# Performance work log

Measured on AMD Instinct MI355X. Metric: run time of the kernel, lower is better.

The kernel has to match this reference:

```python
import jax, jax.numpy as jnp
import numpy as np

H = 12
D_MODEL = 768
D_K = D_MODEL // H  # 64


def setup_inputs() -> dict:
    key = jax.random.key(0)
    ks = jax.random.split(key, 16)
    B, S, D = 4, 1024, D_MODEL
    scale = 1.0 / np.sqrt(D)
    inp = {
        "query": jax.random.normal(ks[0], (B, S, D), jnp.float32),
        "key": jax.random.normal(ks[1], (B, S, D), jnp.float32),
        "value": jax.random.normal(ks[2], (B, S, D), jnp.float32),
        "times": jax.random.normal(ks[3], (2, B, S, D), jnp.float32),
        # learned params (Linear weights stored torch-style [out, in])
        "Wq": jax.random.normal(ks[4], (D, D), jnp.float32) * scale,
        "bq": jnp.zeros((D,), jnp.float32),
        "Wk": jax.random.normal(ks[5], (D, D), jnp.float32) * scale,
        "bk": jnp.zeros((D,), jnp.float32),
        "Wv": jax.random.normal(ks[6], (D, D), jnp.float32) * scale,
        "bv": jnp.zeros((D,), jnp.float32),
        "Wt": jax.random.normal(ks[7], (D, D), jnp.float32) * scale,
        "bt": jnp.zeros((D,), jnp.float32),
        "Wo": jax.random.normal(ks[8], (D, D), jnp.float32) * scale,
        "bo": jnp.zeros((D,), jnp.float32),
    }
    return inp


def _split_heads(x, B, S):
    # [B,S,D] -> [B,H,S,D_K]
    return x.reshape(B, S, H, D_K).transpose(0, 2, 1, 3)


def reference(query, key, value, times, Wq, bq, Wk, bk, Wv, bv, Wt, bt, Wo, bo):
    B, S, D = query.shape
    inv_sqrt_dk = 1.0 / jnp.sqrt(jnp.asarray(D_K, query.dtype))
    # q/k/v projections are identical across time-loop iterations; hoist them.
    q = _split_heads(query @ Wq.T + bq, B, S)   # [B,H,S,dk]
    k = _split_heads(key @ Wk.T + bk, B, S)
    v = _split_heads(value @ Wv.T + bv, B, S)
    x = jnp.zeros_like(q)
    n_times = times.shape[0]
    for i in range(n_times):  # small fixed loop over time embeddings
        t = _split_heads(times[i] @ Wt.T + bt, B, S)
        # dual-score attention: query.time + query.key, each scaled by 1/sqrt(d_k)
        scores = (jnp.einsum('bhqd,bhkd->bhqk', q, t)
                  + jnp.einsum('bhqd,bhkd->bhqk', q, k)) * inv_sqrt_dk
        p = jax.nn.softmax(scores, axis=-1)
        x = x + jnp.einsum('bhqk,bhkd->bhqd', p, v)
    x = x.transpose(0, 2, 1, 3).reshape(B, S, H * D_K)
    return x @ Wo.T + bo
```

## Files before the change

### kernel.cpp

```cpp
#include <hip/hip_runtime.h>
#include <hip/hip_fp16.h>

typedef _Float16 v8h __attribute__((ext_vector_type(8)));
typedef _Float16 v4h __attribute__((ext_vector_type(4)));
typedef _Float16 v2h __attribute__((ext_vector_type(2)));
typedef float v4f __attribute__((ext_vector_type(4)));

#define MFMA_F16 __builtin_amdgcn_mfma_f32_16x16x32_f16
#define EXP2F __builtin_amdgcn_exp2f

__device__ static inline v2h pkrtz(float a, float b) {
  return __builtin_bit_cast(v2h, __builtin_amdgcn_cvt_pkrtz(a, b));
}

__device__ static inline void async_copy16(const void* g, void* l) {
  __builtin_amdgcn_global_load_lds(
      (const __attribute__((address_space(1))) void*)g,
      (__attribute__((address_space(3))) void*)l, 16, 0, 0);
}

struct CastArgs {
  const float* src[5];
  _Float16* dst[5];
  int start[6];
  float scale[5];
};
__global__ void cast_all(CastArgs a) {
  const int g = blockIdx.x * 256 + threadIdx.x;
  if (g >= a.start[5]) return;
  int z = 0;
  #pragma unroll
  for (int i = 1; i < 5; ++i) if (g >= a.start[i]) z = i;
  const int i0 = g - a.start[z];
  const float sc = a.scale[z];
  const float* s = a.src[z] + (size_t)i0 * 8;
  const float4 f0 = *(const float4*)s;
  const float4 f1 = *(const float4*)(s + 4);
  v8h o = {(_Float16)(f0.x * sc), (_Float16)(f0.y * sc),
           (_Float16)(f0.z * sc), (_Float16)(f0.w * sc),
           (_Float16)(f1.x * sc), (_Float16)(f1.y * sc),
           (_Float16)(f1.z * sc), (_Float16)(f1.w * sc)};
  *(v8h*)(a.dst[z] + (size_t)i0 * 8) = o;
}

struct GemmArgs {
  const void* A1[4]; const void* A2[4];
  const _Float16* W1[4]; const _Float16* W2[4];
  const float* b1[4];    const float* b2[4];
  void* out[4];
  float bscale[4];
  int K[4];
  int mode[4];
};

template <int MT, bool AF32>
__global__ __launch_bounds__(256) void gemm_mt(GemmArgs g) {
  constexpr int NMT = MT / 32;
  constexpr int ASLOT = MT / 32;
  __shared__ _Float16 a_lds[(AF32 ? 1 : 2) * MT * 64];
  __shared__ _Float16 w_lds[2 * 128 * 64];
  const int z = blockIdx.z;
  const int KK = g.K[z];
  const int tid = threadIdx.x;
  const int w = tid >> 6, lane = tid & 63, quad = lane >> 4, l16 = lane & 15;
  const int m0 = blockIdx.x * MT, n0 = blockIdx.y * 128;
  const int wm = (w >> 1) * (MT / 2), wn = (w & 1) * 64;

  size_t srcOffW[4]; int ldsOffW[4];
  #pragma unroll
  for (int i = 0; i < 4; ++i) {
    const int c = i * 256 + tid, row = c >> 3, slot = c & 7;
    srcOffW[i] = (size_t)row * 768 + (size_t)((slot ^ (row & 7)) * 8);
    ldsOffW[i] = (i * 256 + w * 64) * 8;
  }

  auto stageW = [&](const _Float16* Wsrc, int kc, int buf) {
    #pragma unroll
    for (int i = 0; i < 4; ++i)
      async_copy16(Wsrc + (size_t)n0 * 768 + kc + srcOffW[i],
                   &w_lds[buf * 8192 + ldsOffW[i]]);
  };
  auto stageA16 = [&](const _Float16* Asrc, int kc, int buf) {
    #pragma unroll
    for (int i = 0; i < MT / 32; ++i)
      async_copy16(Asrc + (size_t)m0 * 768 + kc + srcOffW[i],
                   &a_lds[buf * MT * 64 + ldsOffW[i]]);
  };

  int rowA[ASLOT], colA[ASLOT], dstA[ASLOT];
  float4 areg[ASLOT][2];
  if constexpr (AF32) {
    #pragma unroll
    for (int i = 0; i < ASLOT; ++i) {
      const int s = i * 256 + tid, row = s >> 3, slot = s & 7;
      rowA[i] = row;
      colA[i] = (slot ^ (row & 7)) * 8;
      dstA[i] = s * 8;
    }
  }
  auto loadA = [&](const float* Af, int kc) {
    #pragma unroll
    for (int i = 0; i < ASLOT; ++i) {
      const float* p = Af + (size_t)(m0 + rowA[i]) * 768 + kc + colA[i];
      areg[i][0] = *(const float4*)p;
      areg[i][1] = *(const float4*)(p + 4);
    }
  };
  auto writeA = [&]() {
    #pragma unroll
    for (int i = 0; i < ASLOT; ++i) {
      const float4 f0 = areg[i][0], f1 = areg[i][1];
      v8h o = {(_Float16)f0.x, (_Float16)f0.y, (_Float16)f0.z, (_Float16)f0.w,
               (_Float16)f1.x, (_Float16)f1.y, (_Float16)f1.z, (_Float16)f1.w};
      *(v8h*)&a_lds[dstA[i]] = o;
    }
  };

  const void* A1 = g.A1[z]; const void* A2 = g.A2[z];
  const _Float16* W1 = g.W1[z]; const _Float16* W2 = g.W2[z];

  v4f acc[NMT][4] = {};

  if constexpr (AF32) loadA((const float*)A1, 0);
  else stageA16((const _Float16*)A1, 0, 0);
  stageW(W1, 0, 0);

  int cur = 0;
  for (int k0 = 0; k0 < KK; k0 += 64) {
    const int k0n = k0 + 64;
    const bool has_next = k0n < KK;
    const int kcn = (k0n < 768) ? k0n : k0n - 768;
    const bool nfirst = k0n < 768;

    __syncthreads();

    if constexpr (AF32) {
      writeA();
      __syncthreads();
      if (has_next) {
        loadA((const float*)(nfirst ? A1 : A2), kcn);
        stageW(nfirst ? W1 : W2, kcn, cur ^ 1);
      }
    } else {
      if (has_next) {
        stageA16((const _Float16*)(nfirst ? A1 : A2), kcn, cur ^ 1);
        stageW(nfirst ? W1 : W2, kcn, cur ^ 1);
      }
    }

    const _Float16* al;
    if constexpr (AF32) al = a_lds; else al = &a_lds[cur * MT * 64];
    const _Float16* wl = &w_lds[cur * 8192];

    #pragma unroll
    for (int kh = 0; kh < 2; ++kh) {
      v8h af[NMT], bf[4];
      #pragma unroll
      for (int mt = 0; mt < NMT; ++mt) {
        const int r = wm + mt * 16 + l16;
        af[mt] = *(const v8h*)&al[r * 64 + (((kh * 4 + quad) ^ (r & 7)) * 8)];
      }
      #pragma unroll
      for (int nt = 0; nt < 4; ++nt) {
        const int r = wn + nt * 16 + l16;
        bf[nt] = *(const v8h*)&wl[r * 64 + (((kh * 4 + quad) ^ (r & 7)) * 8)];
      }
      #pragma unroll
      for (int mt = 0; mt < NMT; ++mt)
        #pragma unroll
        for (int nt = 0; nt < 4; ++nt)
          acc[mt][nt] = MFMA_F16(af[mt], bf[nt], acc[mt][nt], 0, 0, 0);
    }
    cur ^= 1;
  }

  const int mode = g.mode[z];
  #pragma unroll
  for (int nt = 0; nt < 4; ++nt) {
    const int col = n0 + wn + nt * 16 + l16;
    float bv = g.b1[z][col] * g.bscale[z];
    if (g.b2[z]) bv += g.b2[z][col];
    if (mode == 1) {
      _Float16* outp = (_Float16*)g.out[z];
      const int h = col >> 6, dk = col & 63;
      #pragma unroll
      for (int mt = 0; mt < NMT; ++mt) {
        const int row = m0 + wm + mt * 16 + quad * 4;
        const int b = row >> 10, s = row & 1023;
        const int sp = (s & ~31) | ((s & 12) << 1) | ((s & 16) >> 2);
        v4h pack = {(_Float16)(acc[mt][nt][0] + bv), (_Float16)(acc[mt][nt][1] + bv),
                    (_Float16)(acc[mt][nt][2] + bv), (_Float16)(acc[mt][nt][3] + bv)};
        *(v4h*)&outp[(size_t)((b * 12 + h) * 64 + dk) * 1024 + sp] = pack;
      }
    } else {
      #pragma unroll
      for (int mt = 0; mt < NMT; ++mt)
        #pragma unroll
        for (int r = 0; r < 4; ++r) {
          const int row = m0 + wm + mt * 16 + quad * 4 + r;
          const float v = acc[mt][nt][r] + bv;
          if (mode == 2) ((float*)g.out[z])[(size_t)row * 768 + col] = v;
          else ((_Float16*)g.out[z])[(size_t)row * 768 + col] = (_Float16)v;
        }
    }
  }
}

__global__ __launch_bounds__(256) void attn(
    const _Float16* __restrict__ Q,
    const _Float16* __restrict__ KT0, const _Float16* __restrict__ KT1,
    const _Float16* __restrict__ Vt,
    _Float16* __restrict__ X)
{
  __shared__ _Float16 lds[6 * 4096];

  const int tid = threadIdx.x;
  const int w = tid >> 6, lane = tid & 63, quad = lane >> 4, l16 = lane & 15;

  const int orig = blockIdx.y * 16 + blockIdx.x;
  const int wgid = (orig & 7) * 96 + (orig >> 3);
  const int bh = wgid >> 4, q0 = (wgid & 15) * 64;
  const int b = bh / 12, h = bh % 12;
  const size_t base = (size_t)b * 1024 * 768 + h * 64;

  const _Float16* k0s = KT0 + base;
  const _Float16* k1s = KT1 + base;
  const _Float16* vs  = Vt + (size_t)bh * 64 * 1024;

  size_t ktOff[2], vOff[2]; int ldsOff[2];
  #pragma unroll
  for (int i = 0; i < 2; ++i) {
    const int c = i * 256 + w * 64 + lane, row = c >> 3, slot = c & 7;
    const int logical = slot ^ (row & 7);
    ktOff[i] = (size_t)row * 768 + (size_t)(logical * 8);
    vOff[i] = (size_t)row * 1024 + (size_t)(logical * 8);
    ldsOff[i] = c * 8;
  }
  auto stage = [&](int buf) {
    #pragma unroll
    for (int i = 0; i < 2; ++i) {
      async_copy16(k0s + ktOff[i], &lds[buf * 4096 + ldsOff[i]]);
      async_copy16(k1s + ktOff[i], &lds[8192 + buf * 4096 + ldsOff[i]]);
      async_copy16(vs + vOff[i], &lds[16384 + buf * 4096 + ldsOff[i]]);
    }
    k0s += 64 * 768; k1s += 64 * 768; vs += 64;
  };

  const _Float16* Qw = Q + base + (size_t)(q0 + w * 16) * 768;
  const v8h qf0 = *(const v8h*)(Qw + (size_t)l16 * 768 + quad * 8);
  const v8h qf1 = *(const v8h*)(Qw + (size_t)l16 * 768 + 32 + quad * 8);

  int ra0[4], ra1[4];
  #pragma unroll
  for (int t = 0; t < 4; ++t) {
    const int r = t * 16 + l16, rw = r & 7;
    ra0[t] = (r * 64 + ((quad ^ rw) * 8)) * 2;
    ra1[t] = ra0[t] ^ 64;
  }

  const _Float16 one = (_Float16)1.f;
  const v8h ones8 = {one, one, one, one, one, one, one, one};
  v4f o[2][4] = {};
  v4f osum[2] = {};

  auto body = [&](int B, bool doStage) {
    __syncthreads();
    if (doStage) stage((B == 0) ? 1 : 0);

    const char* L = (const char*)lds;

    v4f s[2][4];
    __builtin_amdgcn_s_setprio(1);
    #pragma unroll
    for (int kvt = 0; kvt < 4; ++kvt) {
      const v8h k00 = *(const v8h*)(L + B + ra0[kvt]);
      const v8h k01 = *(const v8h*)(L + B + ra1[kvt]);
      const v8h k10 = *(const v8h*)(L + 16384 + B + ra0[kvt]);
      const v8h k11 = *(const v8h*)(L + 16384 + B + ra1[kvt]);
      s[0][kvt] = MFMA_F16(k00, qf0, v4f{}, 0, 0, 0);
      s[0][kvt] = MFMA_F16(k01, qf1, s[0][kvt], 0, 0, 0);
      s[1][kvt] = MFMA_F16(k10, qf0, v4f{}, 0, 0, 0);
      s[1][kvt] = MFMA_F16(k11, qf1, s[1][kvt], 0, 0, 0);
    }
    __builtin_amdgcn_s_setprio(0);

    v8h pb8[2][2];
    #pragma unroll
    for (int t = 0; t < 2; ++t)
      #pragma unroll
      for (int gg = 0; gg < 2; ++gg) {
        const v4f sa = s[t][gg * 2], sb = s[t][gg * 2 + 1];
        const v2h a0 = pkrtz(EXP2F(sa[0]), EXP2F(sa[1]));
        const v2h a1 = pkrtz(EXP2F(sa[2]), EXP2F(sa[3]));
        const v2h b0 = pkrtz(EXP2F(sb[0]), EXP2F(sb[1]));
        const v2h b1 = pkrtz(EXP2F(sb[2]), EXP2F(sb[3]));
        pb8[t][gg] = v8h{a0[0], a0[1], a1[0], a1[1], b0[0], b0[1], b1[0], b1[1]};
        osum[t] = MFMA_F16(ones8, pb8[t][gg], osum[t], 0, 0, 0);
      }

    __builtin_amdgcn_s_setprio(1);
    #pragma unroll
    for (int dkt = 0; dkt < 4; ++dkt) {
      const v8h v0 = *(const v8h*)(L + 32768 + B + ra0[dkt]);
      const v8h v1 = *(const v8h*)(L + 32768 + B + ra1[dkt]);
      o[0][dkt] = MFMA_F16(v0, pb8[0][0], o[0][dkt], 0, 0, 0);
      o[0][dkt] = MFMA_F16(v1, pb8[0][1], o[0][dkt], 0, 0, 0);
      o[1][dkt] = MFMA_F16(v0, pb8[1][0], o[1][dkt], 0, 0, 0);
      o[1][dkt] = MFMA_F16(v1, pb8[1][1], o[1][dkt], 0, 0, 0);
    }
    __builtin_amdgcn_s_setprio(0);
  };

  stage(0);
  for (int it = 0; it < 7; ++it) {
    body(0, true);
    body(8192, true);
  }
  body(0, true);
  body(8192, false);

  const float i0 = 1.0f / osum[0][0], i1 = 1.0f / osum[1][0];

  _Float16* Xw = X + base + (size_t)(q0 + w * 16 + l16) * 768;
  #pragma unroll
  for (int dkt = 0; dkt < 4; ++dkt) {
    v4h pack;
    #pragma unroll
    for (int r = 0; r < 4; ++r)
      pack[r] = (_Float16)(o[0][dkt][r] * i0 + o[1][dkt][r] * i1);
    *(v4h*)&Xw[dkt * 16 + quad * 4] = pack;
  }
}

extern "C" void kernel_launch(void* const* d_in, const int* in_sizes, int n_in,
                              void* d_out, int out_size, void* d_ws, size_t ws_size,
                              hipStream_t stream) {
  const float* query = (const float*)d_in[0];
  const float* key   = (const float*)d_in[1];
  const float* value = (const float*)d_in[2];
  const float* times = (const float*)d_in[3];
  const float* Wq = (const float*)d_in[4];  const float* bq = (const float*)d_in[5];
  const float* Wk = (const float*)d_in[6];  const float* bk = (const float*)d_in[7];
  const float* Wv = (const float*)d_in[8];  const float* bv = (const float*)d_in[9];
  const float* Wt = (const float*)d_in[10]; const float* bt = (const float*)d_in[11];
  const float* Wo = (const float*)d_in[12]; const float* bo = (const float*)d_in[13];
  float* out = (float*)d_out;

  const size_t NELEM = (size_t)4096 * 768;
  const size_t WELEM = (size_t)768 * 768;
  const float QSCALE = 0.125f * 1.4426950408889634f;

  char* ws = (char*)d_ws;
  size_t off = 0;
  auto alloc = [&](size_t bytes) {
    void* p = ws + off; off += (bytes + 255) & ~(size_t)255; return p;
  };
  _Float16* wqh = (_Float16*)alloc(WELEM * 2);
  _Float16* wkh = (_Float16*)alloc(WELEM * 2);
  _Float16* wvh = (_Float16*)alloc(WELEM * 2);
  _Float16* wth = (_Float16*)alloc(WELEM * 2);
  _Float16* woh = (_Float16*)alloc(WELEM * 2);
  _Float16* Qh  = (_Float16*)alloc(NELEM * 2);
  _Float16* KT0 = (_Float16*)alloc(NELEM * 2);
  _Float16* KT1 = (_Float16*)alloc(NELEM * 2);
  _Float16* Vt  = (_Float16*)alloc(NELEM * 2);
  _Float16* Xh  = (_Float16*)alloc(NELEM * 2);

  CastArgs ca = {};
  const int nW8 = (int)(WELEM / 8);
  const float* csrc[5] = {Wq, Wk, Wv, Wt, Wo};
  _Float16* cdst[5] = {wqh, wkh, wvh, wth, woh};
  int acc8 = 0;
  for (int i = 0; i < 5; ++i) {
    ca.src[i] = csrc[i]; ca.dst[i] = cdst[i];
    ca.start[i] = acc8;
    acc8 += nW8;
    ca.scale[i] = (i == 0) ? QSCALE : 1.0f;
  }
  ca.start[5] = acc8;
  cast_all<<<dim3((acc8 + 255) / 256), 256, 0, stream>>>(ca);

  GemmArgs pa = {};
  pa.A1[0] = times;         pa.A2[0] = key; pa.W1[0] = wth; pa.W2[0] = wkh;
  pa.b1[0] = bt; pa.b2[0] = bk; pa.out[0] = KT0; pa.bscale[0] = 1.0f;
  pa.K[0] = 1536; pa.mode[0] = 0;
  pa.A1[1] = times + NELEM; pa.A2[1] = key; pa.W1[1] = wth; pa.W2[1] = wkh;
  pa.b1[1] = bt; pa.b2[1] = bk; pa.out[1] = KT1; pa.bscale[1] = 1.0f;
  pa.K[1] = 1536; pa.mode[1] = 0;
  pa.A1[2] = query; pa.A2[2] = query; pa.W1[2] = wqh; pa.W2[2] = wqh;
  pa.b1[2] = bq; pa.b2[2] = nullptr; pa.out[2] = Qh; pa.bscale[2] = QSCALE;
  pa.K[2] = 768; pa.mode[2] = 0;
  pa.A1[3] = value; pa.A2[3] = value; pa.W1[3] = wvh; pa.W2[3] = wvh;
  pa.b1[3] = bv; pa.b2[3] = nullptr; pa.out[3] = Vt; pa.bscale[3] = 1.0f;
  pa.K[3] = 768; pa.mode[3] = 1;
  gemm_mt<128, true><<<dim3(32, 6, 4), 256, 0, stream>>>(pa);

  attn<<<dim3(16, 48), 256, 0, stream>>>(Qh, KT0, KT1, Vt, Xh);

  GemmArgs oa = {};
  oa.A1[0] = Xh; oa.A2[0] = Xh; oa.W1[0] = woh; oa.W2[0] = woh;
  oa.b1[0] = bo; oa.b2[0] = nullptr; oa.out[0] = out; oa.bscale[0] = 1.0f;
  oa.K[0] = 768; oa.mode[0] = 2;
  gemm_mt<64, false><<<dim3(64, 6, 1), 256, 0, stream>>>(oa);
}
```

Before: 218.6 us.

## Split GEMM template into specialized kernels with explicit waitcnt and barrier scheduling

Replaces the templated gemm_mt with two specialized kernels, one for the fp32-input projections and one for the fp16 output projection. Each kernel uses explicit s_waitcnt with partial vmcnt, raw s_barrier, and sched_barrier fences so the next tile's global loads can stay in flight across the barrier. Each kernel also raises wave priority around the MFMA block. The goal is to cut synchronization stalls and overlap memory with compute. In exchange, correctness now depends on hand-counted vmcnt values matching the number of loads issued per stage.

```diff
diff --git a/kernel.cpp b/kernel.cpp
--- a/kernel.cpp
+++ b/kernel.cpp
@@ -8,6 +8,7 @@
 
 #define MFMA_F16 __builtin_amdgcn_mfma_f32_16x16x32_f16
 #define EXP2F __builtin_amdgcn_exp2f
+#define SCHED_FENCE() __builtin_amdgcn_sched_barrier(0)
 
 __device__ static inline v2h pkrtz(float a, float b) {
   return __builtin_bit_cast(v2h, __builtin_amdgcn_cvt_pkrtz(a, b));
@@ -53,127 +54,10 @@
   int mode[4];
 };
 
-template <int MT, bool AF32>
-__global__ __launch_bounds__(256) void gemm_mt(GemmArgs g) {
-  constexpr int NMT = MT / 32;
-  constexpr int ASLOT = MT / 32;
-  __shared__ _Float16 a_lds[(AF32 ? 1 : 2) * MT * 64];
-  __shared__ _Float16 w_lds[2 * 128 * 64];
-  const int z = blockIdx.z;
-  const int KK = g.K[z];
-  const int tid = threadIdx.x;
-  const int w = tid >> 6, lane = tid & 63, quad = lane >> 4, l16 = lane & 15;
-  const int m0 = blockIdx.x * MT, n0 = blockIdx.y * 128;
-  const int wm = (w >> 1) * (MT / 2), wn = (w & 1) * 64;
-
-  size_t srcOffW[4]; int ldsOffW[4];
-  #pragma unroll
-  for (int i = 0; i < 4; ++i) {
-    const int c = i * 256 + tid, row = c >> 3, slot = c & 7;
-    srcOffW[i] = (size_t)row * 768 + (size_t)((slot ^ (row & 7)) * 8);
-    ldsOffW[i] = (i * 256 + w * 64) * 8;
-  }
-
-  auto stageW = [&](const _Float16* Wsrc, int kc, int buf) {
-    #pragma unroll
-    for (int i = 0; i < 4; ++i)
-      async_copy16(Wsrc + (size_t)n0 * 768 + kc + srcOffW[i],
-                   &w_lds[buf * 8192 + ldsOffW[i]]);
-  };
-  auto stageA16 = [&](const _Float16* Asrc, int kc, int buf) {
-    #pragma unroll
-    for (int i = 0; i < MT / 32; ++i)
-      async_copy16(Asrc + (size_t)m0 * 768 + kc + srcOffW[i],
-                   &a_lds[buf * MT * 64 + ldsOffW[i]]);
-  };
-
-  int rowA[ASLOT], colA[ASLOT], dstA[ASLOT];
-  float4 areg[ASLOT][2];
-  if constexpr (AF32) {
-    #pragma unroll
-    for (int i = 0; i < ASLOT; ++i) {
-      const int s = i * 256 + tid, row = s >> 3, slot = s & 7;
-      rowA[i] = row;
-      colA[i] = (slot ^ (row & 7)) * 8;
-      dstA[i] = s * 8;
-    }
-  }
-  auto loadA = [&](const float* Af, int kc) {
-    #pragma unroll
-    for (int i = 0; i < ASLOT; ++i) {
-      const float* p = Af + (size_t)(m0 + rowA[i]) * 768 + kc + colA[i];
-      areg[i][0] = *(const float4*)p;
-      areg[i][1] = *(const float4*)(p + 4);
-    }
-  };
-  auto writeA = [&]() {
-    #pragma unroll
-    for (int i = 0; i < ASLOT; ++i) {
-      const float4 f0 = areg[i][0], f1 = areg[i][1];
-      v8h o = {(_Float16)f0.x, (_Float16)f0.y, (_Float16)f0.z, (_Float16)f0.w,
-               (_Float16)f1.x, (_Float16)f1.y, (_Float16)f1.z, (_Float16)f1.w};
-      *(v8h*)&a_lds[dstA[i]] = o;
-    }
-  };
-
-  const void* A1 = g.A1[z]; const void* A2 = g.A2[z];
-  const _Float16* W1 = g.W1[z]; const _Float16* W2 = g.W2[z];
-
-  v4f acc[NMT][4] = {};
-
-  if constexpr (AF32) loadA((const float*)A1, 0);
-  else stageA16((const _Float16*)A1, 0, 0);
-  stageW(W1, 0, 0);
-
-  int cur = 0;
-  for (int k0 = 0; k0 < KK; k0 += 64) {
-    const int k0n = k0 + 64;
-    const bool has_next = k0n < KK;
-    const int kcn = (k0n < 768) ? k0n : k0n - 768;
-    const bool nfirst = k0n < 768;
-
-    __syncthreads();
-
-    if constexpr (AF32) {
-      writeA();
-      __syncthreads();
-      if (has_next) {
-        loadA((const float*)(nfirst ? A1 : A2), kcn);
-        stageW(nfirst ? W1 : W2, kcn, cur ^ 1);
-      }
-    } else {
-      if (has_next) {
-        stageA16((const _Float16*)(nfirst ? A1 : A2), kcn, cur ^ 1);
-        stageW(nfirst ? W1 : W2, kcn, cur ^ 1);
-      }
-    }
-
-    const _Float16* al;
-    if constexpr (AF32) al = a_lds; else al = &a_lds[cur * MT * 64];
-    const _Float16* wl = &w_lds[cur * 8192];
-
-    #pragma unroll
-    for (int kh = 0; kh < 2; ++kh) {
-      v8h af[NMT], bf[4];
-      #pragma unroll
-      for (int mt = 0; mt < NMT; ++mt) {
-        const int r = wm + mt * 16 + l16;
-        af[mt] = *(const v8h*)&al[r * 64 + (((kh * 4 + quad) ^ (r & 7)) * 8)];
-      }
-      #pragma unroll
-      for (int nt = 0; nt < 4; ++nt) {
-        const int r = wn + nt * 16 + l16;
-        bf[nt] = *(const v8h*)&wl[r * 64 + (((kh * 4 + quad) ^ (r & 7)) * 8)];
-      }
-      #pragma unroll
-      for (int mt = 0; mt < NMT; ++mt)
-        #pragma unroll
-        for (int nt = 0; nt < 4; ++nt)
-          acc[mt][nt] = MFMA_F16(af[mt], bf[nt], acc[mt][nt], 0, 0, 0);
-    }
-    cur ^= 1;
-  }
-
+template <int NMT>
+__device__ static inline void gemm_epilogue(const GemmArgs& g, int z,
+                                            v4f (&acc)[NMT][4], int m0, int n0,
+                                            int wm, int wn, int quad, int l16) {
   const int mode = g.mode[z];
   #pragma unroll
   for (int nt = 0; nt < 4; ++nt) {
@@ -204,6 +88,190 @@
         }
     }
   }
+}
+
+__global__ __launch_bounds__(256) void gemm_proj(GemmArgs g) {
+  __shared__ _Float16 a_lds[128 * 64];
+  __shared__ _Float16 w_lds[2 * 128 * 64];
+  const int z = blockIdx.z;
+  const int KK = g.K[z];
+  const int tid = threadIdx.x;
+  const int w = tid >> 6, lane = tid & 63, quad = lane >> 4, l16 = lane & 15;
+  const int m0 = blockIdx.x * 128, n0 = blockIdx.y * 128;
+  const int wm = (w >> 1) * 64, wn = (w & 1) * 64;
+
+  size_t srcOffW[4]; int ldsOffW[4];
+  #pragma unroll
+  for (int i = 0; i < 4; ++i) {
+    const int c = i * 256 + tid, row = c >> 3, slot = c & 7;
+    srcOffW[i] = (size_t)row * 768 + (size_t)((slot ^ (row & 7)) * 8);
+    ldsOffW[i] = (i * 256 + w * 64) * 8;
+  }
+  auto stageW = [&](const _Float16* Wsrc, int kc, int buf) {
+    #pragma unroll
+    for (int i = 0; i < 4; ++i)
+      async_copy16(Wsrc + (size_t)n0 * 768 + kc + srcOffW[i],
+                   &w_lds[buf * 8192 + ldsOffW[i]]);
+  };
+
+  int rowA[4], colA[4], dstA[4];
+  float4 areg[4][2];
+  #pragma unroll
+  for (int i = 0; i < 4; ++i) {
+    const int s = i * 256 + tid, row = s >> 3, slot = s & 7;
+    rowA[i] = row;
+    colA[i] = (slot ^ (row & 7)) * 8;
+    dstA[i] = s * 8;
+  }
+  auto loadA = [&](const float* Af, int kc) {
+    #pragma unroll
+    for (int i = 0; i < 4; ++i) {
+      const float* p = Af + (size_t)(m0 + rowA[i]) * 768 + kc + colA[i];
+      areg[i][0] = *(const float4*)p;
+      areg[i][1] = *(const float4*)(p + 4);
+    }
+  };
+  auto writeA = [&]() {
+    #pragma unroll
+    for (int i = 0; i < 4; ++i) {
+      const float4 f0 = areg[i][0], f1 = areg[i][1];
+      v8h o = {(_Float16)f0.x, (_Float16)f0.y, (_Float16)f0.z, (_Float16)f0.w,
+               (_Float16)f1.x, (_Float16)f1.y, (_Float16)f1.z, (_Float16)f1.w};
+      *(v8h*)&a_lds[dstA[i]] = o;
+    }
+  };
+
+  const void* A1 = g.A1[z]; const void* A2 = g.A2[z];
+  const _Float16* W1 = g.W1[z]; const _Float16* W2 = g.W2[z];
+
+  v4f acc[4][4] = {};
+
+  loadA((const float*)A1, 0);
+  stageW(W1, 0, 0);
+
+  for (int k0 = 0; k0 < KK; k0 += 64) {
+    const int cur = (k0 >> 6) & 1;
+    const int k0n = k0 + 64;
+    const bool hn = k0n < KK;
+    const int kcn = (k0n < 768) ? k0n : k0n - 768;
+    const bool nf = k0n < 768;
+
+    writeA();
+    if (hn) {
+      loadA((const float*)(nf ? A1 : A2), kcn);
+      stageW(nf ? W1 : W2, kcn, cur ^ 1);
+    }
+    SCHED_FENCE();
+    if (hn) asm volatile("s_waitcnt vmcnt(12) lgkmcnt(0)" ::: "memory");
+    else    asm volatile("s_waitcnt vmcnt(0) lgkmcnt(0)" ::: "memory");
+    SCHED_FENCE();
+    __builtin_amdgcn_s_barrier();
+    SCHED_FENCE();
+
+    const _Float16* wl = &w_lds[cur * 8192];
+    #pragma unroll
+    for (int kh = 0; kh < 2; ++kh) {
+      v8h af[4], bf[4];
+      #pragma unroll
+      for (int mt = 0; mt < 4; ++mt) {
+        const int r = wm + mt * 16 + l16;
+        af[mt] = *(const v8h*)&a_lds[r * 64 + (((kh * 4 + quad) ^ (r & 7)) * 8)];
+      }
+      #pragma unroll
+      for (int nt = 0; nt < 4; ++nt) {
+        const int r = wn + nt * 16 + l16;
+        bf[nt] = *(const v8h*)&wl[r * 64 + (((kh * 4 + quad) ^ (r & 7)) * 8)];
+      }
+      __builtin_amdgcn_s_setprio(1);
+      #pragma unroll
+      for (int mt = 0; mt < 4; ++mt)
+        #pragma unroll
+        for (int nt = 0; nt < 4; ++nt)
+          acc[mt][nt] = MFMA_F16(af[mt], bf[nt], acc[mt][nt], 0, 0, 0);
+      __builtin_amdgcn_s_setprio(0);
+    }
+    SCHED_FENCE();
+    __builtin_amdgcn_s_barrier();
+    SCHED_FENCE();
+  }
+
+  gemm_epilogue<4>(g, z, acc, m0, n0, wm, wn, quad, l16);
+}
+
+__global__ __launch_bounds__(256) void gemm_out(GemmArgs g) {
+  __shared__ _Float16 a_lds[2 * 64 * 64];
+  __shared__ _Float16 w_lds[2 * 128 * 64];
+  const int z = 0;
+  const int KK = g.K[z];
+  const int tid = threadIdx.x;
+  const int w = tid >> 6, lane = tid & 63, quad = lane >> 4, l16 = lane & 15;
+  const int m0 = blockIdx.x * 64, n0 = blockIdx.y * 128;
+  const int wm = (w >> 1) * 32, wn = (w & 1) * 64;
+
+  size_t srcOffW[4]; int ldsOffW[4];
+  #pragma unroll
+  for (int i = 0; i < 4; ++i) {
+    const int c = i * 256 + tid, row = c >> 3, slot = c & 7;
+    srcOffW[i] = (size_t)row * 768 + (size_t)((slot ^ (row & 7)) * 8);
+    ldsOffW[i] = (i * 256 + w * 64) * 8;
+  }
+  const _Float16* A1 = (const _Float16*)g.A1[z];
+  const _Float16* W1 = g.W1[z];
+
+  auto stage = [&](int kc, int buf) {
+    #pragma unroll
+    for (int i = 0; i < 2; ++i)
+      async_copy16(A1 + (size_t)m0 * 768 + kc + srcOffW[i],
+                   &a_lds[buf * 4096 + ldsOffW[i]]);
+    #pragma unroll
+    for (int i = 0; i < 4; ++i)
+      async_copy16(W1 + (size_t)n0 * 768 + kc + srcOffW[i],
+                   &w_lds[buf * 8192 + ldsOffW[i]]);
+  };
+
+  v4f acc[2][4] = {};
+  stage(0, 0);
+
+  for (int k0 = 0; k0 < KK; k0 += 64) {
+    const int cur = (k0 >> 6) & 1;
+    const bool hn = k0 + 64 < KK;
+    if (hn) stage(k0 + 64, cur ^ 1);
+    SCHED_FENCE();
+    if (hn) asm volatile("s_waitcnt vmcnt(6) lgkmcnt(0)" ::: "memory");
+    else    asm volatile("s_waitcnt vmcnt(0) lgkmcnt(0)" ::: "memory");
+    SCHED_FENCE();
+    __builtin_amdgcn_s_barrier();
+    SCHED_FENCE();
+
+    const _Float16* al = &a_lds[cur * 4096];
+    const _Float16* wl = &w_lds[cur * 8192];
+    #pragma unroll
+    for (int kh = 0; kh < 2; ++kh) {
+      v8h af[2], bf[4];
+      #pragma unroll
+      for (int mt = 0; mt < 2; ++mt) {
+        const int r = wm + mt * 16 + l16;
+        af[mt] = *(const v8h*)&al[r * 64 + (((kh * 4 + quad) ^ (r & 7)) * 8)];
+      }
+      #pragma unroll
+      for (int nt = 0; nt < 4; ++nt) {
+        const int r = wn + nt * 16 + l16;
+        bf[nt] = *(const v8h*)&wl[r * 64 + (((kh * 4 + quad) ^ (r & 7)) * 8)];
+      }
+      __builtin_amdgcn_s_setprio(1);
+      #pragma unroll
+      for (int mt = 0; mt < 2; ++mt)
+        #pragma unroll
+        for (int nt = 0; nt < 4; ++nt)
+          acc[mt][nt] = MFMA_F16(af[mt], bf[nt], acc[mt][nt], 0, 0, 0);
+      __builtin_amdgcn_s_setprio(0);
+    }
+    SCHED_FENCE();
+    __builtin_amdgcn_s_barrier();
+    SCHED_FENCE();
+  }
+
+  gemm_epilogue<2>(g, z, acc, m0, n0, wm, wn, quad, l16);
 }
 
 __global__ __launch_bounds__(256) void attn(
@@ -393,7 +461,7 @@
   pa.A1[3] = value; pa.A2[3] = value; pa.W1[3] = wvh; pa.W2[3] = wvh;
   pa.b1[3] = bv; pa.b2[3] = nullptr; pa.out[3] = Vt; pa.bscale[3] = 1.0f;
   pa.K[3] = 768; pa.mode[3] = 1;
-  gemm_mt<128, true><<<dim3(32, 6, 4), 256, 0, stream>>>(pa);
+  gemm_proj<<<dim3(32, 6, 4), 256, 0, stream>>>(pa);
 
   attn<<<dim3(16, 48), 256, 0, stream>>>(Qh, KT0, KT1, Vt, Xh);
 
@@ -401,5 +469,5 @@
   oa.A1[0] = Xh; oa.A2[0] = Xh; oa.W1[0] = woh; oa.W2[0] = woh;
   oa.b1[0] = bo; oa.b2[0] = nullptr; oa.out[0] = out; oa.bscale[0] = 1.0f;
   oa.K[0] = 768; oa.mode[0] = 2;
-  gemm_mt<64, false><<<dim3(64, 6, 1), 256, 0, stream>>>(oa);
-}
+  gemm_out<<<dim3(64, 6, 1), 256, 0, stream>>>(oa);
+}
```

After: 215.7 us. About the same (-1.3%).
